# Kernel optimization log

Hardware: AMD Instinct MI355X
Metric: run time of the kernel (lower is better)

## Reference

```python
import jax, jax.numpy as jnp
import numpy as np

HEADS = 16
GROUPS = 4
C_IN = 1024
C_OUT = 1024


def att_linear(x, w, b):
    # x: [B,S,C_in], w: [G, C_in/G, C_out/G], b: [C_out]
    B, S, _ = x.shape
    xg = x.reshape(B, S, GROUPS, C_IN // GROUPS)
    out = jnp.einsum('bsgi,gio->bsgo', xg, w).reshape(B, S, C_OUT)
    return out + b


def restricted_softmax(score, margin=0.0):
    # clamp row max at 0, add exp(margin - max) margin term to denominator
    smax = jnp.maximum(jnp.max(score, axis=-1, keepdims=True), 0.0)
    e = jnp.exp(score - smax)
    return e / (jnp.sum(e, axis=-1, keepdims=True) + jnp.exp(margin - smax))


def setup_inputs() -> dict:
    key = jax.random.key(0)
    ks = jax.random.split(key, 9)
    B, S = 4, 1024
    dpg_in, dpg_out = C_IN // GROUPS, C_OUT // GROUPS
    wscale = 1.0 / np.sqrt(dpg_in)
    return {
        'query': jax.random.normal(ks[0], (B, S, C_IN), jnp.float32),
        'key': jax.random.normal(ks[1], (B, S, C_IN), jnp.float32),
        'value': jax.random.normal(ks[2], (B, S, C_IN), jnp.float32),
        'wq': jax.random.uniform(ks[3], (GROUPS, dpg_in, dpg_out), jnp.float32, -wscale, wscale),
        'bq': jax.random.uniform(ks[4], (C_OUT,), jnp.float32, -wscale, wscale),
        'wk': jax.random.uniform(ks[5], (GROUPS, dpg_in, dpg_out), jnp.float32, -wscale, wscale),
        'bk': jax.random.uniform(ks[6], (C_OUT,), jnp.float32, -wscale, wscale),
        'wv': jax.random.uniform(ks[7], (GROUPS, dpg_in, dpg_out), jnp.float32, -wscale, wscale),
        'bv': jax.random.uniform(ks[8], (C_OUT,), jnp.float32, -wscale, wscale),
    }


def reference(query, key, value, wq, bq, wk, bk, wv, bv):
    B, S, _ = query.shape
    d = C_OUT // HEADS
    q = att_linear(query, wq, bq).reshape(B, S, HEADS, d).transpose(0, 2, 1, 3)
    k = att_linear(key, wk, bk).reshape(B, S, HEADS, d).transpose(0, 2, 1, 3)
    v = att_linear(value, wv, bv).reshape(B, S, HEADS, d).transpose(0, 2, 1, 3)
    score = jnp.einsum('bhqd,bhkd->bhqk', q, k) / jnp.sqrt(jnp.float32(d))
    attn = restricted_softmax(score)  # dropout p=0
    out = jnp.einsum('bhqk,bhkd->bhqd', attn, v)
    return out.transpose(0, 2, 1, 3).reshape(B, S, C_OUT)
```

## Files before the change

kernel.cpp:

```cpp
#include <hip/hip_runtime.h>
#include <hip/hip_bf16.h>

#define HEADS   16
#define GROUPS  4
#define C_IN    1024
#define C_OUT   1024
#define BATCH   4
#define SEQ     1024
#define DHEAD   64
#define DPG     256
#define MROWS   (BATCH * SEQ)
#define NBH     (BATCH * HEADS)
#define W_ELEMS ((size_t)GROUPS * DPG * DPG)
#define N_ELEMS ((size_t)NBH * SEQ * DHEAD)

typedef short  bhalf8  __attribute__((ext_vector_type(8)));
typedef short  short4v __attribute__((ext_vector_type(4)));
typedef float  f32x4   __attribute__((ext_vector_type(4)));
typedef unsigned short ushort8v __attribute__((ext_vector_type(8)));

#define MFMA16 __builtin_amdgcn_mfma_f32_16x16x32_bf16

__device__ __forceinline__ unsigned short f2bf(float x) {
    union { __hip_bfloat16 b; unsigned short u; } c;
    c.b = __float2bfloat16(x);
    return c.u;
}
__device__ __forceinline__ float bf2f(unsigned short s) {
    return __uint_as_float(((unsigned int)s) << 16);
}
__device__ __forceinline__ float exp2a(float x) {
    float r;
    asm("v_exp_f32 %0, %1" : "=v"(r) : "v"(x));
    return r;
}

__device__ __forceinline__ void gload16(const void* gsrc, void* lds) {
    __builtin_amdgcn_global_load_lds(
        (const __attribute__((address_space(1))) unsigned int*)(unsigned long long)(uintptr_t)gsrc,
        (__attribute__((address_space(3))) unsigned int*)(unsigned int)(uintptr_t)lds,
        16, 0, 0);
}

__global__ void wsplit(const float* __restrict__ w0,
                       const float* __restrict__ w1,
                       const float* __restrict__ w2,
                       unsigned short* __restrict__ wtbase)
{
    const int tid = threadIdx.x;
    const int kt = blockIdx.x, ot = blockIdx.y;
    const int which = blockIdx.z >> 2, g = blockIdx.z & 3;
    const float* w = (which == 0) ? w0 : (which == 1) ? w1 : w2;
    unsigned short* wth = wtbase + (size_t)which * 2 * W_ELEMS;
    unsigned short* wtl = wth + W_ELEMS;

    __shared__ float Ls[64][68];
    const float* wg = w + (size_t)g * DPG * DPG;
#pragma unroll
    for (int p = 0; p < 4; ++p) {
        const int kk = 16 * p + (tid >> 4);
        const int oo = 4 * (tid & 15);
        const float4 v = *reinterpret_cast<const float4*>(
            wg + (size_t)(kt * 64 + kk) * DPG + ot * 64 + oo);
        Ls[kk][oo + 0] = v.x; Ls[kk][oo + 1] = v.y;
        Ls[kk][oo + 2] = v.z; Ls[kk][oo + 3] = v.w;
    }
    __syncthreads();
    unsigned short* th = wth + (size_t)g * DPG * DPG;
    unsigned short* tl = wtl + (size_t)g * DPG * DPG;
#pragma unroll
    for (int p = 0; p < 4; ++p) {
        const int oo = 16 * p + (tid >> 4);
        const int k4 = 4 * (tid & 15);
        ushort4 hv, lv;
        {
            float v0 = Ls[k4 + 0][oo], v1 = Ls[k4 + 1][oo];
            float v2 = Ls[k4 + 2][oo], v3 = Ls[k4 + 3][oo];
            hv.x = f2bf(v0); lv.x = f2bf(v0 - bf2f(hv.x));
            hv.y = f2bf(v1); lv.y = f2bf(v1 - bf2f(hv.y));
            hv.z = f2bf(v2); lv.z = f2bf(v2 - bf2f(hv.z));
            hv.w = f2bf(v3); lv.w = f2bf(v3 - bf2f(hv.w));
        }
        const size_t o = (size_t)(ot * 64 + oo) * DPG + kt * 64 + k4;
        *reinterpret_cast<ushort4*>(th + o) = hv;
        *reinterpret_cast<ushort4*>(tl + o) = lv;
    }
}

__launch_bounds__(256, 2)
__global__ void proj_mfma(const float* __restrict__ xq,
                          const float* __restrict__ xk,
                          const float* __restrict__ xv,
                          const unsigned short* __restrict__ wtbase,
                          const float* __restrict__ bq,
                          const float* __restrict__ bk,
                          const float* __restrict__ bv,
                          unsigned short* __restrict__ outbase)
{
    const int tid  = threadIdx.x;
    const int wave = tid >> 6;
    const int lane = tid & 63;
    const int h    = lane >> 4;
    const int ln   = lane & 15;
    const int mq   = wave >> 1;
    const int nq   = wave & 1;
    const int bx   = blockIdx.x;
    const int by   = blockIdx.y;
    const int which = blockIdx.z >> 2, g = blockIdx.z & 3;
    const int m0   = bx * 64;

    const float* x    = (which == 0) ? xq : (which == 1) ? xk : xv;
    const float* bias = (which == 0) ? bq : (which == 1) ? bk : bv;
    unsigned short* outh = outbase + (size_t)which * 2 * N_ELEMS;
    unsigned short* outl = outh + N_ELEMS;

    __shared__ uint4 smem4[3072];
    char* sp = (char*)smem4;

    f32x4 acc[2][4];
#pragma unroll
    for (int a = 0; a < 2; ++a)
#pragma unroll
        for (int b = 0; b < 4; ++b) acc[a][b] = (f32x4){0.f, 0.f, 0.f, 0.f};

    const float* xg = x + (size_t)m0 * C_IN + g * DPG;
    const unsigned short* wh = wtbase + (size_t)which * 2 * W_ELEMS
                             + ((size_t)g * DPG + by * 128) * DPG;
    const unsigned short* wl = wh + W_ELEMS;

    int b_goff[4], b_lds[4];
#pragma unroll
    for (int c = 0; c < 4; ++c) {
        const int o  = (c * 4 + wave) * 1024 + lane * 16;
        const int rw = o >> 7;
        const int kidx = ((o & 127) ^ ((rw & 7) << 4)) >> 1;
        b_goff[c] = rw * DPG + kidx;
        b_lds[c]  = (c * 4 + wave) * 1024;
    }

    const int arb = tid >> 4, ac = tid & 15;

    for (int it = 0; it < 4; ++it) {
        const int k0 = it * 64;
        if (it > 0) __syncthreads();
#pragma unroll
        for (int c = 0; c < 4; ++c) {
            gload16(wh + b_goff[c] + k0, sp + 16384 + b_lds[c]);
            gload16(wl + b_goff[c] + k0, sp + 32768 + b_lds[c]);
        }
#pragma unroll
        for (int p = 0; p < 4; ++p) {
            const int rr = 16 * p + arb;
            const float4 v = *reinterpret_cast<const float4*>(
                xg + (size_t)rr * C_IN + k0 + 4 * ac);
            ushort4 hv, lv;
            hv.x = f2bf(v.x); lv.x = f2bf(v.x - bf2f(hv.x));
            hv.y = f2bf(v.y); lv.y = f2bf(v.y - bf2f(hv.y));
            hv.z = f2bf(v.z); lv.z = f2bf(v.z - bf2f(hv.z));
            hv.w = f2bf(v.w); lv.w = f2bf(v.w - bf2f(hv.w));
            const int off = (8 * ac) ^ ((rr & 7) << 4);
            *reinterpret_cast<ushort4*>(sp + rr * 128 + off) = hv;
            *reinterpret_cast<ushort4*>(sp + 8192 + rr * 128 + off) = lv;
        }
        __syncthreads();

#pragma unroll
        for (int kk = 0; kk < 2; ++kk) {
            bhalf8 ah[2], al[2], bh_[4], bl_[4];
#pragma unroll
            for (int mt = 0; mt < 2; ++mt) {
                const int row = 32 * mq + 16 * mt + ln;
                const int off = (64 * kk + 16 * h) ^ ((row & 7) << 4);
                ah[mt] = *reinterpret_cast<const bhalf8*>(sp + row * 128 + off);
                al[mt] = *reinterpret_cast<const bhalf8*>(sp + 8192 + row * 128 + off);
            }
#pragma unroll
            for (int nt = 0; nt < 4; ++nt) {
                const int row = 64 * nq + 16 * nt + ln;
                const int off = (64 * kk + 16 * h) ^ ((row & 7) << 4);
                bh_[nt] = *reinterpret_cast<const bhalf8*>(sp + 16384 + row * 128 + off);
                bl_[nt] = *reinterpret_cast<const bhalf8*>(sp + 32768 + row * 128 + off);
            }
#pragma unroll
            for (int mt = 0; mt < 2; ++mt)
#pragma unroll
                for (int nt = 0; nt < 4; ++nt) {
                    acc[mt][nt] = MFMA16(ah[mt], bh_[nt], acc[mt][nt], 0, 0, 0);
                    acc[mt][nt] = MFMA16(al[mt], bh_[nt], acc[mt][nt], 0, 0, 0);
                    acc[mt][nt] = MFMA16(ah[mt], bl_[nt], acc[mt][nt], 0, 0, 0);
                }
        }
    }
    __syncthreads();

    const int hd = g * 4 + by * 2 + nq;
    const int b  = bx >> 4;
    const size_t bhb = ((size_t)b * HEADS + hd) * (SEQ * DHEAD);
    const int wbase = wave * 8192;
    const int sg0 = (bx & 15) * 64 + 32 * mq;
    const float oscale = (which == 0) ? 0.18033688011112042f : 1.0f;
    float bnt[4];
#pragma unroll
    for (int nt = 0; nt < 4; ++nt)
        bnt[nt] = bias[g * 256 + by * 128 + 64 * nq + 16 * nt + ln];

    if (which != 2) {
#pragma unroll
        for (int mt = 0; mt < 2; ++mt)
#pragma unroll
            for (int nt = 0; nt < 4; ++nt)
#pragma unroll
                for (int r = 0; r < 4; ++r) {
                    const int sl = 16 * mt + 4 * h + r;
                    const float v = (acc[mt][nt][r] + bnt[nt]) * oscale;
                    const unsigned short hh = f2bf(v);
                    const unsigned short ll = f2bf(v - bf2f(hh));
                    const int cb = (2 * (16 * nt + ln)) ^ ((sl & 7) << 4);
                    *reinterpret_cast<unsigned short*>(sp + wbase + sl * 128 + cb) = hh;
                    *reinterpret_cast<unsigned short*>(sp + wbase + 4096 + sl * 128 + cb) = ll;
                }
        __syncthreads();
#pragma unroll
        for (int p = 0; p < 4; ++p) {
            const int sl = 8 * p + (lane >> 3);
            const int cb = (16 * (lane & 7)) ^ ((sl & 7) << 4);
            const size_t go = bhb + (size_t)(sg0 + sl) * 64 + 8 * (lane & 7);
            *reinterpret_cast<ushort8v*>(outh + go) =
                *reinterpret_cast<const ushort8v*>(sp + wbase + sl * 128 + cb);
            *reinterpret_cast<ushort8v*>(outl + go) =
                *reinterpret_cast<const ushort8v*>(sp + wbase + 4096 + sl * 128 + cb);
        }
    } else {
#pragma unroll
        for (int mt = 0; mt < 2; ++mt)
#pragma unroll
            for (int nt = 0; nt < 4; ++nt) {
                const int dl = 16 * nt + ln;
                ushort4 hv, lv;
                {
                    float v0 = acc[mt][nt][0] + bnt[nt];
                    float v1 = acc[mt][nt][1] + bnt[nt];
                    float v2 = acc[mt][nt][2] + bnt[nt];
                    float v3 = acc[mt][nt][3] + bnt[nt];
                    hv.x = f2bf(v0); lv.x = f2bf(v0 - bf2f(hv.x));
                    hv.y = f2bf(v1); lv.y = f2bf(v1 - bf2f(hv.y));
                    hv.z = f2bf(v2); lv.z = f2bf(v2 - bf2f(hv.z));
                    hv.w = f2bf(v3); lv.w = f2bf(v3 - bf2f(hv.w));
                }
                const int off = (32 * mt + 8 * h) ^ ((dl & 7) << 3);
                *reinterpret_cast<ushort4*>(sp + wbase + dl * 64 + off) = hv;
                *reinterpret_cast<ushort4*>(sp + wbase + 4096 + dl * 64 + off) = lv;
            }
        __syncthreads();
#pragma unroll
        for (int p = 0; p < 4; ++p) {
            const int dl  = 16 * p + (lane >> 2);
            const int c16 = 16 * (lane & 3);
            const int o0b = (c16) ^ ((dl & 7) << 3);
            const int o1b = (c16 + 8) ^ ((dl & 7) << 3);
            const size_t go = bhb + (size_t)dl * SEQ + sg0 + 8 * (lane & 3);
            *reinterpret_cast<ushort4*>(outh + go) =
                *reinterpret_cast<const ushort4*>(sp + wbase + dl * 64 + o0b);
            *reinterpret_cast<ushort4*>(outh + go + 4) =
                *reinterpret_cast<const ushort4*>(sp + wbase + dl * 64 + o1b);
            *reinterpret_cast<ushort4*>(outl + go) =
                *reinterpret_cast<const ushort4*>(sp + wbase + 4096 + dl * 64 + o0b);
            *reinterpret_cast<ushort4*>(outl + go + 4) =
                *reinterpret_cast<const ushort4*>(sp + wbase + 4096 + dl * 64 + o1b);
        }
    }
}

__launch_bounds__(256, 3)
__global__ void attn_mfma(const unsigned short* __restrict__ qh,
                          const unsigned short* __restrict__ ql,
                          const unsigned short* __restrict__ kh,
                          const unsigned short* __restrict__ kl,
                          const unsigned short* __restrict__ vth,
                          const unsigned short* __restrict__ vtl,
                          float* __restrict__ out)
{
    const int tid  = threadIdx.x;
    const int wave = tid >> 6;
    const int lane = tid & 63;
    const int h    = lane >> 4;
    const int ln   = lane & 15;
    const int bh   = blockIdx.x;
    const int q0   = blockIdx.y * 128 + wave * 32;

    const size_t bhbase = (size_t)bh * (SEQ * DHEAD);
    const unsigned short* qhp = qh + bhbase;
    const unsigned short* qlp = ql + bhbase;
    const unsigned short* khp = kh + bhbase;
    const unsigned short* klp = kl + bhbase;
    const unsigned short* vhp = vth + bhbase;
    const unsigned short* vlp = vtl + bhbase;

    __shared__ uint4 smem4[3072];
    char* sb = (char*)smem4;

    bhalf8 Qf[2][2][2];
#pragma unroll
    for (int nt = 0; nt < 2; ++nt)
#pragma unroll
        for (int dt = 0; dt < 2; ++dt) {
            const size_t o = (size_t)(q0 + 16 * nt + ln) * DHEAD + dt * 32 + 8 * h;
            Qf[nt][dt][0] = *reinterpret_cast<const bhalf8*>(qhp + o);
            Qf[nt][dt][1] = *reinterpret_cast<const bhalf8*>(qlp + o);
        }

    f32x4 accO[2][4];
#pragma unroll
    for (int a = 0; a < 2; ++a)
#pragma unroll
        for (int b = 0; b < 4; ++b) accO[a][b] = (f32x4){0.f, 0.f, 0.f, 0.f};
    float m_i[2] = {0.f, 0.f};
    float l_i[2] = {1.f, 1.f};

    int rw_[2], kd_[2], lofs_[2];
#pragma unroll
    for (int c = 0; c < 2; ++c) {
        const int o = (c * 4 + wave) * 1024 + lane * 16;
        rw_[c]   = o >> 7;
        kd_[c]   = ((o & 127) ^ ((rw_[c] & 7) << 4)) >> 1;
        lofs_[c] = (c * 4 + wave) * 1024;
    }

#define STAGE_K(BUF, K0)                                                       \
    do {                                                                       \
        _Pragma("unroll")                                                      \
        for (int c = 0; c < 2; ++c) {                                          \
            char* lb = sb + (BUF) + lofs_[c];                                  \
            gload16(khp + (size_t)((K0) + rw_[c]) * DHEAD + kd_[c], lb);       \
            gload16(klp + (size_t)((K0) + rw_[c]) * DHEAD + kd_[c], lb + 8192);\
        }                                                                      \
    } while (0)
#define STAGE_V(K0)                                                            \
    do {                                                                       \
        _Pragma("unroll")                                                      \
        for (int c = 0; c < 2; ++c) {                                          \
            char* lb = sb + 32768 + lofs_[c];                                  \
            gload16(vhp + (size_t)rw_[c] * SEQ + (K0) + kd_[c], lb);           \
            gload16(vlp + (size_t)rw_[c] * SEQ + (K0) + kd_[c], lb + 8192);    \
        }                                                                      \
    } while (0)

    STAGE_K(0, 0);

    for (int t = 0; t < 16; ++t) {
        STAGE_V(t * 64);
        STAGE_K(((t + 1) & 1) * 16384, ((t + 1) & 15) * 64);
        asm volatile("s_waitcnt vmcnt(8)\n\ts_barrier" ::: "memory");

        const char* cb = sb + (t & 1) * 16384;

        f32x4 s_[2][4];
#pragma unroll
        for (int a = 0; a < 2; ++a)
#pragma unroll
            for (int b = 0; b < 4; ++b) s_[a][b] = (f32x4){0.f, 0.f, 0.f, 0.f};
#pragma unroll
        for (int mt = 0; mt < 4; ++mt) {
            const int rr = 16 * mt + ln;
            const int sw = (rr & 7) << 4;
            const bhalf8 Ah0 = *reinterpret_cast<const bhalf8*>(cb + rr * 128 + ((16 * h) ^ sw));
            const bhalf8 Ah1 = *reinterpret_cast<const bhalf8*>(cb + rr * 128 + ((64 + 16 * h) ^ sw));
            const bhalf8 Al0 = *reinterpret_cast<const bhalf8*>(cb + 8192 + rr * 128 + ((16 * h) ^ sw));
            const bhalf8 Al1 = *reinterpret_cast<const bhalf8*>(cb + 8192 + rr * 128 + ((64 + 16 * h) ^ sw));
#pragma unroll
            for (int nt = 0; nt < 2; ++nt) {
                s_[nt][mt] = MFMA16(Ah0, Qf[nt][0][0], s_[nt][mt], 0, 0, 0);
                s_[nt][mt] = MFMA16(Ah1, Qf[nt][1][0], s_[nt][mt], 0, 0, 0);
                s_[nt][mt] = MFMA16(Ah0, Qf[nt][0][1], s_[nt][mt], 0, 0, 0);
                s_[nt][mt] = MFMA16(Ah1, Qf[nt][1][1], s_[nt][mt], 0, 0, 0);
                s_[nt][mt] = MFMA16(Al0, Qf[nt][0][0], s_[nt][mt], 0, 0, 0);
                s_[nt][mt] = MFMA16(Al1, Qf[nt][1][0], s_[nt][mt], 0, 0, 0);
            }
        }

        float Pv[2][4][4];
        bhalf8 Pfh[2][2], Pfl[2][2];
#pragma unroll
        for (int nt = 0; nt < 2; ++nt) {
            float mloc = -1e30f;
#pragma unroll
            for (int mt = 0; mt < 4; ++mt)
#pragma unroll
                for (int rr = 0; rr < 4; ++rr) {
                    const float v = s_[nt][mt][rr];
                    Pv[nt][mt][rr] = v;
                    mloc = fmaxf(mloc, v);
                }
            mloc = fmaxf(mloc, __shfl_xor(mloc, 16));
            mloc = fmaxf(mloc, __shfl_xor(mloc, 32));
            if (__any(mloc > m_i[nt] + 10.0f)) {
                const float mn = fmaxf(m_i[nt], mloc);
                const float sf = exp2a(m_i[nt] - mn);
                m_i[nt] = mn;
                l_i[nt] *= sf;
#pragma unroll
                for (int rr = 0; rr < 4; ++rr) {
                    const float sf_b = __shfl(sf, 20 * h + rr);
#pragma unroll
                    for (int ntd = 0; ntd < 4; ++ntd) accO[nt][ntd][rr] *= sf_b;
                }
            }
            float rs = 0.f;
            const float mcur = m_i[nt];
#pragma unroll
            for (int mt = 0; mt < 4; ++mt)
#pragma unroll
                for (int rr = 0; rr < 4; ++rr) {
                    const float p = exp2a(Pv[nt][mt][rr] - mcur);
                    Pv[nt][mt][rr] = p;
                    rs += p;
                }
            rs += __shfl_xor(rs, 16);
            rs += __shfl_xor(rs, 32);
            l_i[nt] += rs;
#pragma unroll
            for (int kt = 0; kt < 2; ++kt) {
                bhalf8 fh, fl;
#pragma unroll
                for (int j = 0; j < 8; ++j) {
                    const float p = Pv[nt][2 * kt + (j >> 2)][j & 3];
                    const unsigned short hi = f2bf(p);
                    fh[j] = (short)hi;
                    fl[j] = (short)f2bf(p - bf2f(hi));
                }
                Pfh[nt][kt] = fh;
                Pfl[nt][kt] = fl;
            }
        }

        asm volatile("s_waitcnt vmcnt(4)\n\ts_barrier" ::: "memory");

#pragma unroll
        for (int kt = 0; kt < 2; ++kt) {
#pragma unroll
            for (int ntd = 0; ntd < 4; ++ntd) {
                const int rr = 16 * ntd + ln;
                const int sw = (rr & 7) << 4;
                const int c0 = (64 * kt + 8 * h) ^ sw;
                const int c1 = (64 * kt + 32 + 8 * h) ^ sw;
                union { short4v q[2]; bhalf8 v; } ubh, ubl;
                ubh.q[0] = *reinterpret_cast<const short4v*>(sb + 32768 + rr * 128 + c0);
                ubh.q[1] = *reinterpret_cast<const short4v*>(sb + 32768 + rr * 128 + c1);
                ubl.q[0] = *reinterpret_cast<const short4v*>(sb + 40960 + rr * 128 + c0);
                ubl.q[1] = *reinterpret_cast<const short4v*>(sb + 40960 + rr * 128 + c1);
                const bhalf8 Bh = ubh.v;
                const bhalf8 Bl = ubl.v;
#pragma unroll
                for (int nt = 0; nt < 2; ++nt) {
                    accO[nt][ntd] = MFMA16(Pfh[nt][kt], Bh, accO[nt][ntd], 0, 0, 0);
                    accO[nt][ntd] = MFMA16(Pfh[nt][kt], Bl, accO[nt][ntd], 0, 0, 0);
                    accO[nt][ntd] = MFMA16(Pfl[nt][kt], Bh, accO[nt][ntd], 0, 0, 0);
                }
            }
        }
        asm volatile("s_barrier" ::: "memory");
    }
    asm volatile("s_waitcnt vmcnt(0)" ::: "memory");

    const int bB = bh >> 4;
    const int hd = bh & 15;
#pragma unroll
    for (int nt = 0; nt < 2; ++nt) {
        float linv[4];
#pragma unroll
        for (int rr = 0; rr < 4; ++rr) linv[rr] = 1.0f / __shfl(l_i[nt], 20 * h + rr);
#pragma unroll
        for (int rr = 0; rr < 4; ++rr) {
            const int q = q0 + 16 * nt + 4 * h + rr;
            float* orow = out + ((size_t)bB * SEQ + q) * C_OUT + hd * DHEAD + ln;
#pragma unroll
            for (int ntd = 0; ntd < 4; ++ntd)
                orow[16 * ntd] = accO[nt][ntd][rr] * linv[rr];
        }
    }
#undef STAGE_K
#undef STAGE_V
}

extern "C" void kernel_launch(void* const* d_in, const int* in_sizes, int n_in,
                              void* d_out, int out_size, void* d_ws, size_t ws_size,
                              hipStream_t stream) {
    const float* query = (const float*)d_in[0];
    const float* key   = (const float*)d_in[1];
    const float* value = (const float*)d_in[2];
    const float* wq    = (const float*)d_in[3];
    const float* bq    = (const float*)d_in[4];
    const float* wk    = (const float*)d_in[5];
    const float* bk    = (const float*)d_in[6];
    const float* wv    = (const float*)d_in[7];
    const float* bv    = (const float*)d_in[8];

    unsigned short* qkv = (unsigned short*)d_ws;
    unsigned short* wts = qkv + 6 * N_ELEMS;

    dim3 blk(256);
    wsplit<<<dim3(4, 4, 12), blk, 0, stream>>>(wq, wk, wv, wts);
    proj_mfma<<<dim3(MROWS / 64, 2, 12), blk, 0, stream>>>(
        query, key, value, wts, bq, bk, bv, qkv);

    attn_mfma<<<dim3(NBH, SEQ / 128), blk, 0, stream>>>(
        qkv, qkv + N_ELEMS, qkv + 2 * N_ELEMS, qkv + 3 * N_ELEMS,
        qkv + 4 * N_ELEMS, qkv + 5 * N_ELEMS, (float*)d_out);
}
```

Baseline: 182.8 us.

## Split attention block into 8 waves of 16 rows, sum row weights via MFMA

```diff
diff --git a/kernel.cpp b/kernel.cpp
--- a/kernel.cpp
+++ b/kernel.cpp
@@ -87,7 +87,7 @@
     }
 }
 
-__launch_bounds__(256, 2)
+__launch_bounds__(256, 3)
 __global__ void proj_mfma(const float* __restrict__ xq,
                           const float* __restrict__ xk,
                           const float* __restrict__ xv,
@@ -271,7 +271,7 @@
     }
 }
 
-__launch_bounds__(256, 3)
+__launch_bounds__(512, 4)
 __global__ void attn_mfma(const unsigned short* __restrict__ qh,
                           const unsigned short* __restrict__ ql,
                           const unsigned short* __restrict__ kh,
@@ -286,7 +286,7 @@
     const int h    = lane >> 4;
     const int ln   = lane & 15;
     const int bh   = blockIdx.x;
-    const int q0   = blockIdx.y * 128 + wave * 32;
+    const int q0   = blockIdx.y * 128 + wave * 16;
 
     const size_t bhbase = (size_t)bh * (SEQ * DHEAD);
     const unsigned short* qhp = qh + bhbase;
@@ -299,50 +299,39 @@
     __shared__ uint4 smem4[3072];
     char* sb = (char*)smem4;
 
-    bhalf8 Qf[2][2][2];
-#pragma unroll
-    for (int nt = 0; nt < 2; ++nt)
-#pragma unroll
-        for (int dt = 0; dt < 2; ++dt) {
-            const size_t o = (size_t)(q0 + 16 * nt + ln) * DHEAD + dt * 32 + 8 * h;
-            Qf[nt][dt][0] = *reinterpret_cast<const bhalf8*>(qhp + o);
-            Qf[nt][dt][1] = *reinterpret_cast<const bhalf8*>(qlp + o);
-        }
-
-    f32x4 accO[2][4];
-#pragma unroll
-    for (int a = 0; a < 2; ++a)
-#pragma unroll
-        for (int b = 0; b < 4; ++b) accO[a][b] = (f32x4){0.f, 0.f, 0.f, 0.f};
-    float m_i[2] = {0.f, 0.f};
-    float l_i[2] = {1.f, 1.f};
-
-    int rw_[2], kd_[2], lofs_[2];
-#pragma unroll
-    for (int c = 0; c < 2; ++c) {
-        const int o = (c * 4 + wave) * 1024 + lane * 16;
-        rw_[c]   = o >> 7;
-        kd_[c]   = ((o & 127) ^ ((rw_[c] & 7) << 4)) >> 1;
-        lofs_[c] = (c * 4 + wave) * 1024;
-    }
-
-#define STAGE_K(BUF, K0)                                                       \
-    do {                                                                       \
-        _Pragma("unroll")                                                      \
-        for (int c = 0; c < 2; ++c) {                                          \
-            char* lb = sb + (BUF) + lofs_[c];                                  \
-            gload16(khp + (size_t)((K0) + rw_[c]) * DHEAD + kd_[c], lb);       \
-            gload16(klp + (size_t)((K0) + rw_[c]) * DHEAD + kd_[c], lb + 8192);\
-        }                                                                      \
+    const bhalf8 ONES = {0x3F80, 0x3F80, 0x3F80, 0x3F80,
+                         0x3F80, 0x3F80, 0x3F80, 0x3F80};
+
+    bhalf8 Qf[2][2];
+#pragma unroll
+    for (int dt = 0; dt < 2; ++dt) {
+        const size_t o = (size_t)(q0 + ln) * DHEAD + dt * 32 + 8 * h;
+        Qf[dt][0] = *reinterpret_cast<const bhalf8*>(qhp + o);
+        Qf[dt][1] = *reinterpret_cast<const bhalf8*>(qlp + o);
+    }
+
+    f32x4 accO[4];
+#pragma unroll
+    for (int b = 0; b < 4; ++b) accO[b] = (f32x4){0.f, 0.f, 0.f, 0.f};
+    f32x4 accL = (f32x4){1.f, 1.f, 1.f, 1.f};
+    float m_i = 0.f;
+
+    const int o_   = wave * 1024 + lane * 16;
+    const int rw_  = o_ >> 7;
+    const int kd_  = ((o_ & 127) ^ ((rw_ & 7) << 4)) >> 1;
+    const int lofs = wave * 1024;
+
+#define STAGE_K(BUF, K0)                                                   \
+    do {                                                                   \
+        char* lb = sb + (BUF) + lofs;                                      \
+        gload16(khp + (size_t)((K0) + rw_) * DHEAD + kd_, lb);             \
+        gload16(klp + (size_t)((K0) + rw_) * DHEAD + kd_, lb + 8192);      \
     } while (0)
-#define STAGE_V(K0)                                                            \
-    do {                                                                       \
-        _Pragma("unroll")                                                      \
-        for (int c = 0; c < 2; ++c) {                                          \
-            char* lb = sb + 32768 + lofs_[c];                                  \
-            gload16(vhp + (size_t)rw_[c] * SEQ + (K0) + kd_[c], lb);           \
-            gload16(vlp + (size_t)rw_[c] * SEQ + (K0) + kd_[c], lb + 8192);    \
-        }                                                                      \
+#define STAGE_V(K0)                                                        \
+    do {                                                                   \
+        char* lb = sb + 32768 + lofs;                                      \
+        gload16(vhp + (size_t)rw_ * SEQ + (K0) + kd_, lb);                 \
+        gload16(vlp + (size_t)rw_ * SEQ + (K0) + kd_, lb + 8192);          \
     } while (0)
 
     STAGE_K(0, 0);
@@ -350,15 +339,13 @@
     for (int t = 0; t < 16; ++t) {
         STAGE_V(t * 64);
         STAGE_K(((t + 1) & 1) * 16384, ((t + 1) & 15) * 64);
-        asm volatile("s_waitcnt vmcnt(8)\n\ts_barrier" ::: "memory");
+        asm volatile("s_waitcnt vmcnt(4)\n\ts_barrier" ::: "memory");
 
         const char* cb = sb + (t & 1) * 16384;
 
-        f32x4 s_[2][4];
-#pragma unroll
-        for (int a = 0; a < 2; ++a)
-#pragma unroll
-            for (int b = 0; b < 4; ++b) s_[a][b] = (f32x4){0.f, 0.f, 0.f, 0.f};
+        f32x4 s_[4];
+#pragma unroll
+        for (int b = 0; b < 4; ++b) s_[b] = (f32x4){0.f, 0.f, 0.f, 0.f};
 #pragma unroll
         for (int mt = 0; mt < 4; ++mt) {
             const int rr = 16 * mt + ln;
@@ -367,73 +354,66 @@
             const bhalf8 Ah1 = *reinterpret_cast<const bhalf8*>(cb + rr * 128 + ((64 + 16 * h) ^ sw));
             const bhalf8 Al0 = *reinterpret_cast<const bhalf8*>(cb + 8192 + rr * 128 + ((16 * h) ^ sw));
             const bhalf8 Al1 = *reinterpret_cast<const bhalf8*>(cb + 8192 + rr * 128 + ((64 + 16 * h) ^ sw));
-#pragma unroll
-            for (int nt = 0; nt < 2; ++nt) {
-                s_[nt][mt] = MFMA16(Ah0, Qf[nt][0][0], s_[nt][mt], 0, 0, 0);
-                s_[nt][mt] = MFMA16(Ah1, Qf[nt][1][0], s_[nt][mt], 0, 0, 0);
-                s_[nt][mt] = MFMA16(Ah0, Qf[nt][0][1], s_[nt][mt], 0, 0, 0);
-                s_[nt][mt] = MFMA16(Ah1, Qf[nt][1][1], s_[nt][mt], 0, 0, 0);
-                s_[nt][mt] = MFMA16(Al0, Qf[nt][0][0], s_[nt][mt], 0, 0, 0);
-                s_[nt][mt] = MFMA16(Al1, Qf[nt][1][0], s_[nt][mt], 0, 0, 0);
-            }
-        }
-
-        float Pv[2][4][4];
-        bhalf8 Pfh[2][2], Pfl[2][2];
-#pragma unroll
-        for (int nt = 0; nt < 2; ++nt) {
+            s_[mt] = MFMA16(Ah0, Qf[0][0], s_[mt], 0, 0, 0);
+            s_[mt] = MFMA16(Ah1, Qf[1][0], s_[mt], 0, 0, 0);
+            s_[mt] = MFMA16(Ah0, Qf[0][1], s_[mt], 0, 0, 0);
+            s_[mt] = MFMA16(Ah1, Qf[1][1], s_[mt], 0, 0, 0);
+            s_[mt] = MFMA16(Al0, Qf[0][0], s_[mt], 0, 0, 0);
+            s_[mt] = MFMA16(Al1, Qf[1][0], s_[mt], 0, 0, 0);
+        }
+
+        float Pv[4][4];
+        bhalf8 Pfh[2], Pfl[2];
+        {
             float mloc = -1e30f;
 #pragma unroll
             for (int mt = 0; mt < 4; ++mt)
 #pragma unroll
                 for (int rr = 0; rr < 4; ++rr) {
-                    const float v = s_[nt][mt][rr];
-                    Pv[nt][mt][rr] = v;
+                    const float v = s_[mt][rr];
+                    Pv[mt][rr] = v;
                     mloc = fmaxf(mloc, v);
                 }
             mloc = fmaxf(mloc, __shfl_xor(mloc, 16));
             mloc = fmaxf(mloc, __shfl_xor(mloc, 32));
-            if (__any(mloc > m_i[nt] + 10.0f)) {
-                const float mn = fmaxf(m_i[nt], mloc);
-                const float sf = exp2a(m_i[nt] - mn);
-                m_i[nt] = mn;
-                l_i[nt] *= sf;
+            if (__any(mloc > m_i + 10.0f)) {
+                const float mn = fmaxf(m_i, mloc);
+                const float sf = exp2a(m_i - mn);
+                m_i = mn;
 #pragma unroll
                 for (int rr = 0; rr < 4; ++rr) {
                     const float sf_b = __shfl(sf, 20 * h + rr);
-#pragma unroll
-                    for (int ntd = 0; ntd < 4; ++ntd) accO[nt][ntd][rr] *= sf_b;
-                }
-            }
-            float rs = 0.f;
-            const float mcur = m_i[nt];
+                    accL[rr] *= sf_b;
+#pragma unroll
+                    for (int ntd = 0; ntd < 4; ++ntd) accO[ntd][rr] *= sf_b;
+                }
+            }
+            const float mcur = m_i;
 #pragma unroll
             for (int mt = 0; mt < 4; ++mt)
 #pragma unroll
-                for (int rr = 0; rr < 4; ++rr) {
-                    const float p = exp2a(Pv[nt][mt][rr] - mcur);
-                    Pv[nt][mt][rr] = p;
-                    rs += p;
-                }
-            rs += __shfl_xor(rs, 16);
-            rs += __shfl_xor(rs, 32);
-            l_i[nt] += rs;
+                for (int rr = 0; rr < 4; ++rr)
+                    Pv[mt][rr] = exp2a(Pv[mt][rr] - mcur);
 #pragma unroll
             for (int kt = 0; kt < 2; ++kt) {
                 bhalf8 fh, fl;
 #pragma unroll
                 for (int j = 0; j < 8; ++j) {
-                    const float p = Pv[nt][2 * kt + (j >> 2)][j & 3];
+                    const float p = Pv[2 * kt + (j >> 2)][j & 3];
                     const unsigned short hi = f2bf(p);
                     fh[j] = (short)hi;
                     fl[j] = (short)f2bf(p - bf2f(hi));
                 }
-                Pfh[nt][kt] = fh;
-                Pfl[nt][kt] = fl;
-            }
-        }
-
-        asm volatile("s_waitcnt vmcnt(4)\n\ts_barrier" ::: "memory");
+                Pfh[kt] = fh;
+                Pfl[kt] = fl;
+            }
+            accL = MFMA16(Pfh[0], ONES, accL, 0, 0, 0);
+            accL = MFMA16(Pfh[1], ONES, accL, 0, 0, 0);
+            accL = MFMA16(Pfl[0], ONES, accL, 0, 0, 0);
+            accL = MFMA16(Pfl[1], ONES, accL, 0, 0, 0);
+        }
+
+        asm volatile("s_waitcnt vmcnt(2)\n\ts_barrier" ::: "memory");
 
 #pragma unroll
         for (int kt = 0; kt < 2; ++kt) {
@@ -450,12 +430,9 @@
                 ubl.q[1] = *reinterpret_cast<const short4v*>(sb + 40960 + rr * 128 + c1);
                 const bhalf8 Bh = ubh.v;
                 const bhalf8 Bl = ubl.v;
-#pragma unroll
-                for (int nt = 0; nt < 2; ++nt) {
-                    accO[nt][ntd] = MFMA16(Pfh[nt][kt], Bh, accO[nt][ntd], 0, 0, 0);
-                    accO[nt][ntd] = MFMA16(Pfh[nt][kt], Bl, accO[nt][ntd], 0, 0, 0);
-                    accO[nt][ntd] = MFMA16(Pfl[nt][kt], Bh, accO[nt][ntd], 0, 0, 0);
-                }
+                accO[ntd] = MFMA16(Pfh[kt], Bh, accO[ntd], 0, 0, 0);
+                accO[ntd] = MFMA16(Pfh[kt], Bl, accO[ntd], 0, 0, 0);
+                accO[ntd] = MFMA16(Pfl[kt], Bh, accO[ntd], 0, 0, 0);
             }
         }
         asm volatile("s_barrier" ::: "memory");
@@ -465,18 +442,13 @@
     const int bB = bh >> 4;
     const int hd = bh & 15;
 #pragma unroll
-    for (int nt = 0; nt < 2; ++nt) {
-        float linv[4];
-#pragma unroll
-        for (int rr = 0; rr < 4; ++rr) linv[rr] = 1.0f / __shfl(l_i[nt], 20 * h + rr);
-#pragma unroll
-        for (int rr = 0; rr < 4; ++rr) {
-            const int q = q0 + 16 * nt + 4 * h + rr;
-            float* orow = out + ((size_t)bB * SEQ + q) * C_OUT + hd * DHEAD + ln;
-#pragma unroll
-            for (int ntd = 0; ntd < 4; ++ntd)
-                orow[16 * ntd] = accO[nt][ntd][rr] * linv[rr];
-        }
+    for (int rr = 0; rr < 4; ++rr) {
+        const int q = q0 + 4 * h + rr;
+        const float linv = 1.0f / accL[rr];
+        float* orow = out + ((size_t)bB * SEQ + q) * C_OUT + hd * DHEAD + ln;
+#pragma unroll
+        for (int ntd = 0; ntd < 4; ++ntd)
+            orow[16 * ntd] = accO[ntd][rr] * linv;
     }
 #undef STAGE_K
 #undef STAGE_V
@@ -503,7 +475,7 @@
     proj_mfma<<<dim3(MROWS / 64, 2, 12), blk, 0, stream>>>(
         query, key, value, wts, bq, bk, bv, qkv);
 
-    attn_mfma<<<dim3(NBH, SEQ / 128), blk, 0, stream>>>(
+    attn_mfma<<<dim3(NBH, SEQ / 128), dim3(512), 0, stream>>>(
         qkv, qkv + N_ELEMS, qkv + 2 * N_ELEMS, qkv + 3 * N_ELEMS,
         qkv + 4 * N_ELEMS, qkv + 5 * N_ELEMS, (float*)d_out);
 }
```

Result: slower. 188.8 us (+3.3%).
